# Optimization experiments

Measured on AMD Instinct MI355X. Metric: run time of the kernel, lower is better.

## Reference

```python
import math
import jax, jax.numpy as jnp
import numpy as np

N, B, C, H, K = 1024, 8, 512, 8, 5  # seq len, batch, d_model, heads, near_kth
NEG = -1.0e9


def setup_inputs() -> dict:
    key = jax.random.key(0)
    ks = jax.random.split(key, 10)
    s = 0.02
    return {
        "query": jax.random.normal(ks[0], (N, B, C), jnp.float32),
        "key_t": jax.random.normal(ks[1], (N, B, C), jnp.float32),
        "value": jax.random.normal(ks[2], (N, B, C), jnp.float32),
        "src_position": jax.random.normal(ks[3], (N, B, 3), jnp.float32),
        "tgt_position": jax.random.normal(ks[4], (N, B, 3), jnp.float32),
        # nn.MultiheadAttention params (in_proj split into q/k/v, plus out_proj)
        "Wq": jax.random.normal(ks[5], (C, C), jnp.float32) * s,
        "Wk": jax.random.normal(ks[6], (C, C), jnp.float32) * s,
        "Wv": jax.random.normal(ks[7], (C, C), jnp.float32) * s,
        "bq": jnp.zeros((C,), jnp.float32),
        "bk": jnp.zeros((C,), jnp.float32),
        "bv": jnp.zeros((C,), jnp.float32),
        "Wo": jax.random.normal(ks[8], (C, C), jnp.float32) * s,
        "bo": jnp.zeros((C,), jnp.float32),
    }


def reference(query, key_t, value, src_position, tgt_position,
              Wq, Wk, Wv, bq, bk, bv, Wo, bo):
    # --- 'nearby' positional mask ---------------------------------------
    # dist[b, tgt, src] = ||src_position[src,b] - tgt_position[tgt,b]||^2
    diff = src_position[None, :, :, :] - tgt_position[:, None, :, :]  # (Nt,Ns,B,3)
    dist = jnp.sum(diff * diff, axis=-1).transpose(2, 0, 1)           # (B,Nt,Ns)
    # torch: topk(dist, k=5, dim=1, largest=False) -> 5 nearest TARGETS per source
    _, idx = jax.lax.top_k(-dist.transpose(0, 2, 1), K)               # (B,Ns,K) tgt idx
    mask = jnp.full((B, N, N), NEG, jnp.float32)
    b_i = jnp.arange(B)[:, None, None]
    s_i = jnp.arange(N)[None, :, None]
    mask = mask.at[b_i, idx, s_i].set(0.0)                            # (B,Nt,Ns)

    # --- multihead attention (eval mode, dropout=0) ----------------------
    hd = C // H
    scale = 1.0 / math.sqrt(hd)
    q = ((query @ Wq.T + bq) * scale).reshape(N, B, H, hd)
    k = (key_t @ Wk.T + bk).reshape(N, B, H, hd)
    v = (value @ Wv.T + bv).reshape(N, B, H, hd)
    scores = jnp.einsum('tbhd,sbhd->bhts', q, k) + mask[:, None]      # (B,H,Nt,Ns)
    attn = jax.nn.softmax(scores, axis=-1)
    ctx = jnp.einsum('bhts,sbhd->tbhd', attn, v).reshape(N, B, C)
    out = ctx @ Wo.T + bo                                             # (N,B,C)
    attn_avg = attn.mean(axis=1)                                      # (B,Nt,Ns)
    return out, attn_avg
```

## Files before the change

### kernel.cpp

```cpp
#include <hip/hip_runtime.h>
#include <cstdint>
#include <cstddef>

#define NSEQ 1024
#define BATCH 8
#define CMODEL 512
#define NHEAD 8
#define HDIM 64
#define CAP 64
#define FLTMAX 3.402823466e+38f

typedef short bf16x8 __attribute__((ext_vector_type(8)));
typedef float f32x4 __attribute__((ext_vector_type(4)));
typedef unsigned short ushort8v __attribute__((ext_vector_type(8)));
typedef unsigned short ushort2v __attribute__((ext_vector_type(2)));

__device__ inline unsigned short f2bf(float f) {
    unsigned int u = __builtin_bit_cast(unsigned int, f);
    u += 0x7fffu + ((u >> 16) & 1u);
    return (unsigned short)(u >> 16);
}
__device__ inline float bf2f(unsigned short u) {
    return __builtin_bit_cast(float, (unsigned int)u << 16);
}

#define GLDS16(gsrc, ldst) \
    __builtin_amdgcn_global_load_lds((const __attribute__((address_space(1))) void*)(gsrc), \
                                     (__attribute__((address_space(3))) void*)(ldst), 16, 0, 0)

__global__ __launch_bounds__(256) void prep(const float* __restrict__ w0,
                                            const float* __restrict__ w1,
                                            const float* __restrict__ w2,
                                            const float* __restrict__ w3,
                                            const float* __restrict__ value,
                                            const float* __restrict__ tgtp,
                                            const float* __restrict__ srcp,
                                            unsigned short* __restrict__ o0,
                                            unsigned short* __restrict__ o1,
                                            unsigned short* __restrict__ o2,
                                            unsigned short* __restrict__ o3,
                                            unsigned int* __restrict__ zp,
                                            float* __restrict__ vm_raw,
                                            float* __restrict__ tgt_soa,
                                            float* __restrict__ src_soa) {
    const int bid = blockIdx.x;
    const int tid = threadIdx.x;
    if (bid < 512) {
        const int idx = bid * 256 + tid;
        const int seg = idx >> 15;
        const int c   = idx & 32767;
        const float* src = seg == 0 ? w0 : seg == 1 ? w1 : seg == 2 ? w2 : w3;
        unsigned short* dst = seg == 0 ? o0 : seg == 1 ? o1 : seg == 2 ? o2 : o3;
        const float4 v0 = *(const float4*)(src + (size_t)c * 8);
        const float4 v1 = *(const float4*)(src + (size_t)c * 8 + 4);
        ushort8v u;
        u[0] = f2bf(v0.x); u[1] = f2bf(v0.y); u[2] = f2bf(v0.z); u[3] = f2bf(v0.w);
        u[4] = f2bf(v1.x); u[5] = f2bf(v1.y); u[6] = f2bf(v1.z); u[7] = f2bf(v1.w);
        *(ushort8v*)(dst + (size_t)c * 8) = u;
        return;
    }
    if (bid < 544) {
        zp[(bid - 512) * 256 + tid] = 0u;
        return;
    }
    if (bid < 608) {
        const int cb = bid - 544;
        const int b = cb >> 3, cg = cb & 7;
        const int ts = tid >> 6, c = cg * 64 + (tid & 63);
        float s = 0.f;
        for (int i = 0; i < 256; ++i) {
            const int t = ts * 256 + i;
            s += value[((size_t)t * BATCH + b) * CMODEL + c];
        }
        __shared__ float sh[4][64];
        sh[ts][tid & 63] = s;
        __syncthreads();
        if (ts == 0)
            vm_raw[b * CMODEL + c] = sh[0][tid & 63] + sh[1][tid & 63] +
                                     sh[2][tid & 63] + sh[3][tid & 63];
        return;
    }
    const int tb = bid - 608;
    const int which = tb >> 3, b = tb & 7;
    const float* src = which == 0 ? tgtp : srcp;
    float* dst = which == 0 ? tgt_soa : src_soa;
    for (int t = tid; t < NSEQ; t += 256) {
        const float* p = src + ((size_t)t * BATCH + b) * 3;
        dst[(b * 3 + 0) * NSEQ + t] = p[0];
        dst[(b * 3 + 1) * NSEQ + t] = p[1];
        dst[(b * 3 + 2) * NSEQ + t] = p[2];
    }
}

__device__ inline void gemm_fp32A_body(const float* __restrict__ A,
                                       const unsigned short* __restrict__ Wbf,
                                       const float* __restrict__ bias,
                                       unsigned short* __restrict__ outp,
                                       float scale, int m0, int n0) {
    __shared__ __align__(16) unsigned short smem[3 * 8192];
    const int tid = threadIdx.x;
    const int l = tid & 63, w = tid >> 6;
    const int wr = (w >> 1) * 64, wc = (w & 1) * 64;
    const int lr = l & 15, g = l >> 4;

    f32x4 acc[4][4] = {};

    const int rowA = tid >> 2;
    const int slA  = tid & 3;
    const int sw   = (rowA >> 1) & 3;
    const float* aS0 = A + (size_t)(m0 + rowA) * CMODEL + slA * 8;
    const float* aS1 = aS0 + (size_t)64 * CMODEL;
    const int adst0 = rowA * 32 + (slA ^ sw) * 8;
    const int adst1 = adst0 + 64 * 32;
    const unsigned short* bS0 = Wbf + (size_t)(n0 + rowA) * CMODEL + (slA ^ sw) * 8;
    const unsigned short* bS1 = bS0 + (size_t)64 * CMODEL;
    const int wb = w * 512;

    float4 sets[2][4];

    auto LOADA = [&](int S, int k0) {
        sets[S][0] = *(const float4*)(aS0 + k0);
        sets[S][1] = *(const float4*)(aS0 + k0 + 4);
        sets[S][2] = *(const float4*)(aS1 + k0);
        sets[S][3] = *(const float4*)(aS1 + k0 + 4);
    };
    auto CVT_WRITE = [&](int S, int buf) {
        ushort8v u0, u1;
        u0[0] = f2bf(sets[S][0].x); u0[1] = f2bf(sets[S][0].y);
        u0[2] = f2bf(sets[S][0].z); u0[3] = f2bf(sets[S][0].w);
        u0[4] = f2bf(sets[S][1].x); u0[5] = f2bf(sets[S][1].y);
        u0[6] = f2bf(sets[S][1].z); u0[7] = f2bf(sets[S][1].w);
        u1[0] = f2bf(sets[S][2].x); u1[1] = f2bf(sets[S][2].y);
        u1[2] = f2bf(sets[S][2].z); u1[3] = f2bf(sets[S][2].w);
        u1[4] = f2bf(sets[S][3].x); u1[5] = f2bf(sets[S][3].y);
        u1[6] = f2bf(sets[S][3].z); u1[7] = f2bf(sets[S][3].w);
        unsigned short* bb = smem + buf * 8192;
        *(ushort8v*)(bb + adst0) = u0;
        *(ushort8v*)(bb + adst1) = u1;
    };
    auto STAGE_B = [&](int k0, int buf) {
        unsigned short* bb = smem + buf * 8192 + 4096;
        GLDS16(bS0 + k0, bb + wb);
        GLDS16(bS1 + k0, bb + 2048 + wb);
    };
    auto COMPUTE = [&](const unsigned short* base) {
        bf16x8 af[4], bg[4];
        #pragma unroll
        for (int i = 0; i < 4; ++i) {
            const int ra = wr + i * 16 + lr;
            af[i] = *(const bf16x8*)(base + ra * 32 + ((g ^ ((ra >> 1) & 3)) << 3));
        }
        #pragma unroll
        for (int j = 0; j < 4; ++j) {
            const int rb = wc + j * 16 + lr;
            bg[j] = *(const bf16x8*)(base + 4096 + rb * 32 + ((g ^ ((rb >> 1) & 3)) << 3));
        }
        #pragma unroll
        for (int i = 0; i < 4; ++i)
            #pragma unroll
            for (int j = 0; j < 4; ++j)
                acc[i][j] = __builtin_amdgcn_mfma_f32_16x16x32_bf16(af[i], bg[j], acc[i][j], 0, 0, 0);
    };

    LOADA(0, 0);
    LOADA(1, 32);
    STAGE_B(0, 0);
    STAGE_B(32, 1);
    CVT_WRITE(0, 0);
    LOADA(0, 64);

    #pragma unroll
    for (int t = 0; t < 13; ++t) {
        const int S = (t + 1) & 1;
        CVT_WRITE(S, (t + 1) % 3);
        LOADA(S, (t + 3) * 32);
        asm volatile("s_waitcnt vmcnt(10)" ::: "memory");
        asm volatile("s_waitcnt lgkmcnt(0)" ::: "memory");
        __builtin_amdgcn_s_barrier();
        STAGE_B((t + 2) * 32, (t + 2) % 3);
        COMPUTE(smem + (t % 3) * 8192);
    }
    CVT_WRITE(0, 2);
    asm volatile("s_waitcnt vmcnt(6)" ::: "memory");
    asm volatile("s_waitcnt lgkmcnt(0)" ::: "memory");
    __builtin_amdgcn_s_barrier();
    STAGE_B(15 * 32, 0);
    COMPUTE(smem + 1 * 8192);
    CVT_WRITE(1, 0);
    asm volatile("s_waitcnt vmcnt(2)" ::: "memory");
    asm volatile("s_waitcnt lgkmcnt(0)" ::: "memory");
    __builtin_amdgcn_s_barrier();
    COMPUTE(smem + 2 * 8192);
    asm volatile("s_waitcnt vmcnt(0)" ::: "memory");
    asm volatile("s_waitcnt lgkmcnt(0)" ::: "memory");
    __builtin_amdgcn_s_barrier();
    COMPUTE(smem + 0 * 8192);

    #pragma unroll
    for (int i = 0; i < 4; ++i) {
        #pragma unroll
        for (int j = 0; j < 4; ++j) {
            const int col = n0 + wc + j * 16 + lr;
            const float bcol = bias[col];
            #pragma unroll
            for (int r = 0; r < 4; ++r) {
                const int row = m0 + wr + i * 16 + g * 4 + r;
                const float val = (acc[i][j][r] + bcol) * scale;
                const int t = row >> 3, bb = row & 7;
                outp[((size_t)(bb * NSEQ + t)) * CMODEL + col] = f2bf(val);
            }
        }
    }
}

__global__ __launch_bounds__(256, 3) void mega(const float* __restrict__ Aq,
                                               const float* __restrict__ Ak,
                                               const float* __restrict__ Av,
                                               const unsigned short* __restrict__ Wq,
                                               const unsigned short* __restrict__ Wk,
                                               const unsigned short* __restrict__ Wv,
                                               const float* __restrict__ bq,
                                               const float* __restrict__ bk,
                                               const float* __restrict__ bv,
                                               unsigned short* __restrict__ oq,
                                               unsigned short* __restrict__ ok,
                                               unsigned short* __restrict__ ov,
                                               const float* __restrict__ src_soa,
                                               const float* __restrict__ tgt_soa,
                                               int* __restrict__ row_cnt,
                                               int* __restrict__ row_list,
                                               const float* __restrict__ vm_raw,
                                               float* __restrict__ vm) {
    const int p = blockIdx.x;

    if (p < 768) {
        const int logical = (p & 7) * 96 + (p >> 3);
        const int z = logical >> 8;
        const int r = logical & 255;
        const int m0 = (r >> 2) * 128, n0 = (r & 3) * 128;
        const float* A = z == 0 ? Aq : z == 1 ? Ak : Av;
        const unsigned short* W = z == 0 ? Wq : z == 1 ? Wk : Wv;
        const float* bi = z == 0 ? bq : z == 1 ? bk : bv;
        unsigned short* o = z == 0 ? oq : z == 1 ? ok : ov;
        const float sc = z == 0 ? 0.125f : 1.0f;
        gemm_fp32A_body(A, W, bi, o, sc, m0, n0);
        return;
    }

    if (p >= 2816) {
        const int bsel = p - 2816;
        const int c0 = threadIdx.x * 2;
        float s0 = 0.f, s1 = 0.f;
        const unsigned short* w0r = Wv + (size_t)c0 * CMODEL;
        const unsigned short* w1r = w0r + CMODEL;
        const float* vr = vm_raw + bsel * CMODEL;
        for (int k8 = 0; k8 < 64; ++k8) {
            const ushort8v w0 = *(const ushort8v*)(w0r + k8 * 8);
            const ushort8v w1 = *(const ushort8v*)(w1r + k8 * 8);
            const float4 va = *(const float4*)(vr + k8 * 8);
            const float4 vb = *(const float4*)(vr + k8 * 8 + 4);
            s0 += va.x * bf2f(w0[0]) + va.y * bf2f(w0[1]) + va.z * bf2f(w0[2]) + va.w * bf2f(w0[3])
                + vb.x * bf2f(w0[4]) + vb.y * bf2f(w0[5]) + vb.z * bf2f(w0[6]) + vb.w * bf2f(w0[7]);
            s1 += va.x * bf2f(w1[0]) + va.y * bf2f(w1[1]) + va.z * bf2f(w1[2]) + va.w * bf2f(w1[3])
                + vb.x * bf2f(w1[4]) + vb.y * bf2f(w1[5]) + vb.z * bf2f(w1[6]) + vb.w * bf2f(w1[7]);
        }
        vm[bsel * CMODEL + c0]     = s0 * (1.f / (float)NSEQ) + bv[c0];
        vm[bsel * CMODEL + c0 + 1] = s1 * (1.f / (float)NSEQ) + bv[c0 + 1];
        return;
    }

    const int w = threadIdx.x >> 6, lane = threadIdx.x & 63;
    const int wg = (p - 768) * 4 + w;
    const int s = wg & 1023, b = wg >> 10;

    const float* tx = tgt_soa + (b * 3 + 0) * NSEQ;
    const float* ty = tgt_soa + (b * 3 + 1) * NSEQ;
    const float* tz = tgt_soa + (b * 3 + 2) * NSEQ;
    const float sx = src_soa[(b * 3 + 0) * NSEQ + s];
    const float sy = src_soa[(b * 3 + 1) * NSEQ + s];
    const float sz = src_soa[(b * 3 + 2) * NSEQ + s];

    float dv[16];
    #pragma unroll
    for (int i = 0; i < 16; ++i) {
        const int t = i * 64 + lane;
        const float dx = tx[t] - sx;
        const float dy = ty[t] - sy;
        const float dz = tz[t] - sz;
        dv[i] = dx * dx + dy * dy + dz * dz;
    }

    #pragma unroll
    for (int k = 0; k < 5; ++k) {
        float bvv = FLTMAX;
        int   bii = 0x7fffffff;
        #pragma unroll
        for (int i = 0; i < 16; ++i) {
            if (dv[i] < bvv) { bvv = dv[i]; bii = i * 64 + lane; }
        }
        #pragma unroll
        for (int off = 1; off < 64; off <<= 1) {
            const float ov = __shfl_xor(bvv, off);
            const int   oi = __shfl_xor(bii, off);
            if (ov < bvv || (ov == bvv && oi < bii)) { bvv = ov; bii = oi; }
        }
        if (lane == (bii & 63)) {
            #pragma unroll
            for (int i = 0; i < 16; ++i)
                if (bii == i * 64 + lane) dv[i] = FLTMAX;
        }
        if (lane == 0) {
            const int pos = atomicAdd(&row_cnt[b * NSEQ + bii], 1);
            if (pos < CAP) row_list[((size_t)b * NSEQ + bii) * CAP + pos] = s;
        }
    }
}

__global__ __launch_bounds__(256, 3) void gemm_out(const unsigned short* __restrict__ Abf,
                                                   const unsigned short* __restrict__ Wbf,
                                                   const float* __restrict__ bias,
                                                   float* __restrict__ out) {
    __shared__ __align__(16) unsigned short smem[3 * 6144];
    const int p = blockIdx.x;
    const int logical = (p & 7) * 64 + (p >> 3);
    const int m0 = (logical >> 3) * 128, n0 = (logical & 7) * 64;

    const int tid = threadIdx.x;
    const int l = tid & 63, w = tid >> 6;
    const int wr = (w >> 1) * 64, wc = (w & 1) * 32;
    const int lr = l & 15, g = l >> 4;

    f32x4 acc[4][2] = {};

    const int rowX = tid >> 2;
    const int kg0  = (tid & 3) ^ ((rowX >> 1) & 3);
    const unsigned short* aS0 = Abf + (size_t)(m0 + rowX) * CMODEL + kg0 * 8;
    const unsigned short* aS1 = aS0 + (size_t)64 * CMODEL;
    const unsigned short* bS0 = Wbf + (size_t)(n0 + rowX) * CMODEL + kg0 * 8;
    const int wb = w * 512;

    auto STAGE = [&](int k0, int buf) {
        unsigned short* bb = smem + buf * 6144;
        GLDS16(aS0 + k0, bb + wb);
        GLDS16(aS1 + k0, bb + 2048 + wb);
        GLDS16(bS0 + k0, bb + 4096 + wb);
    };
    auto COMPUTE = [&](const unsigned short* base) {
        bf16x8 af[4], bg[2];
        #pragma unroll
        for (int i = 0; i < 4; ++i) {
            const int ra = wr + i * 16 + lr;
            af[i] = *(const bf16x8*)(base + ra * 32 + ((g ^ ((ra >> 1) & 3)) << 3));
        }
        #pragma unroll
        for (int j = 0; j < 2; ++j) {
            const int rb = wc + j * 16 + lr;
            bg[j] = *(const bf16x8*)(base + 4096 + rb * 32 + ((g ^ ((rb >> 1) & 3)) << 3));
        }
        #pragma unroll
        for (int i = 0; i < 4; ++i)
            #pragma unroll
            for (int j = 0; j < 2; ++j)
                acc[i][j] = __builtin_amdgcn_mfma_f32_16x16x32_bf16(af[i], bg[j], acc[i][j], 0, 0, 0);
    };

    STAGE(0, 0);
    STAGE(32, 1);

    int cur = 0;
    for (int t = 0; t < 15; ++t) {
        asm volatile("s_waitcnt vmcnt(3)" ::: "memory");
        __builtin_amdgcn_s_barrier();
        if (t < 14) {
            int nb = cur + 2; if (nb >= 3) nb -= 3;
            STAGE((t + 2) * 32, nb);
        }
        COMPUTE(smem + cur * 6144);
        ++cur; if (cur == 3) cur = 0;
    }
    asm volatile("s_waitcnt vmcnt(0)" ::: "memory");
    __builtin_amdgcn_s_barrier();
    COMPUTE(smem + cur * 6144);

    #pragma unroll
    for (int i = 0; i < 4; ++i) {
        #pragma unroll
        for (int j = 0; j < 2; ++j) {
            const int col = n0 + wc + j * 16 + lr;
            const float bcol = bias[col];
            #pragma unroll
            for (int r = 0; r < 4; ++r) {
                const int row = m0 + wr + i * 16 + g * 4 + r;
                out[(size_t)row * CMODEL + col] = acc[i][j][r] + bcol;
            }
        }
    }
}

__global__ __launch_bounds__(256) void sparse_attn(const unsigned short* __restrict__ q_ws,
                                                   const unsigned short* __restrict__ k_ws,
                                                   const unsigned short* __restrict__ v_ws,
                                                   const int* __restrict__ row_cnt,
                                                   const int* __restrict__ row_list,
                                                   const float* __restrict__ vm,
                                                   unsigned short* __restrict__ ctx,
                                                   float* __restrict__ attn_out) {
    const int t = blockIdx.x;
    const int b = blockIdx.y;
    const int tid = threadIdx.x;

    int cnt = row_cnt[b * NSEQ + t];
    if (cnt > CAP) cnt = CAP;

    float* arow = attn_out + ((size_t)b * NSEQ + t) * NSEQ;

    if (cnt == 0) {
        const float u = 1.f / (float)NSEQ;
        const float4 uv = {u, u, u, u};
        ((float4*)arow)[tid] = uv;
        for (int c = tid; c < CMODEL; c += 256)
            ctx[((size_t)t * BATCH + b) * CMODEL + c] = f2bf(vm[b * CMODEL + c]);
        return;
    }

    {
        const float4 zv = {0.f, 0.f, 0.f, 0.f};
        ((float4*)arow)[tid] = zv;
    }

    __shared__ float qs[CMODEL];
    __shared__ float esc[CAP][8];
    __shared__ float denom[8];
    __shared__ int   slist[CAP];

    if (tid < 8) denom[tid] = 0.f;
    if (tid < cnt) slist[tid] = row_list[((size_t)b * NSEQ + t) * CAP + tid];
    {
        const ushort2v qv = *(const ushort2v*)(q_ws + ((size_t)b * NSEQ + t) * CMODEL + tid * 2);
        qs[tid * 2] = bf2f(qv[0]); qs[tid * 2 + 1] = bf2f(qv[1]);
    }
    __syncthreads();

    const int wid = tid >> 6, lane = tid & 63;
    for (int i = wid; i < cnt; i += 4) {
        const int s = slist[i];
        const ushort8v kv = *(const ushort8v*)(k_ws + ((size_t)b * NSEQ + s) * CMODEL + lane * 8);
        const float* qrow = qs + lane * 8;
        float part = 0.f;
        #pragma unroll
        for (int j = 0; j < 8; ++j) part += qrow[j] * bf2f(kv[j]);
        part += __shfl_xor(part, 1);
        part += __shfl_xor(part, 2);
        part += __shfl_xor(part, 4);
        if ((lane & 7) == 0) {
            const int h = lane >> 3;
            const float e = __expf(part);
            esc[i][h] = e;
            atomicAdd(&denom[h], e);
        }
    }
    __syncthreads();

    for (int x = tid; x < cnt * 8; x += 256)
        esc[x >> 3][x & 7] /= denom[x & 7];
    __syncthreads();

    for (int i = tid; i < cnt; i += 256) {
        float pm = 0.f;
        #pragma unroll
        for (int h = 0; h < 8; ++h) pm += esc[i][h];
        arow[slist[i]] = pm * 0.125f;
    }

    const int c0 = tid * 2;
    const int h0 = c0 >> 6;
    float acc0 = 0.f, acc1 = 0.f;
    for (int i = 0; i < cnt; ++i) {
        const int s = slist[i];
        const float p = esc[i][h0];
        const ushort2v vv = *(const ushort2v*)(v_ws + ((size_t)b * NSEQ + s) * CMODEL + c0);
        acc0 += p * bf2f(vv[0]); acc1 += p * bf2f(vv[1]);
    }
    unsigned short* crow = ctx + ((size_t)t * BATCH + b) * CMODEL;
    ushort2v cv; cv[0] = f2bf(acc0); cv[1] = f2bf(acc1);
    *(ushort2v*)(crow + c0) = cv;
}

extern "C" void kernel_launch(void* const* d_in, const int* in_sizes, int n_in,
                              void* d_out, int out_size, void* d_ws, size_t ws_size,
                              hipStream_t stream) {
    (void)in_sizes; (void)n_in; (void)out_size; (void)ws_size;

    const float* query = (const float*)d_in[0];
    const float* key_t = (const float*)d_in[1];
    const float* value = (const float*)d_in[2];
    const float* srcp  = (const float*)d_in[3];
    const float* tgtp  = (const float*)d_in[4];
    const float* Wq    = (const float*)d_in[5];
    const float* Wk    = (const float*)d_in[6];
    const float* Wv    = (const float*)d_in[7];
    const float* bq    = (const float*)d_in[8];
    const float* bk    = (const float*)d_in[9];
    const float* bv    = (const float*)d_in[10];
    const float* Wo    = (const float*)d_in[11];
    const float* bo    = (const float*)d_in[12];

    float* out      = (float*)d_out;
    float* attn_out = out + (size_t)NSEQ * BATCH * CMODEL;

    const size_t NBC = (size_t)BATCH * NSEQ * CMODEL;
    const size_t WSZ = (size_t)CMODEL * CMODEL;
    unsigned short* q_ws  = (unsigned short*)d_ws;
    unsigned short* k_ws  = q_ws + NBC;
    unsigned short* v_ws  = k_ws + NBC;
    unsigned short* ctxbf = v_ws + NBC;
    unsigned short* wqbf  = ctxbf + NBC;
    unsigned short* wkbf  = wqbf + WSZ;
    unsigned short* wvbf  = wkbf + WSZ;
    unsigned short* wobf  = wvbf + WSZ;
    int*   row_cnt  = (int*)(wobf + WSZ);
    float* vm       = (float*)(row_cnt + BATCH * NSEQ);
    float* vm_raw   = vm + BATCH * CMODEL;
    float* tgt_soa  = vm_raw + BATCH * CMODEL;
    float* src_soa  = tgt_soa + (size_t)BATCH * 3 * NSEQ;
    int*   row_list = (int*)(src_soa + (size_t)BATCH * 3 * NSEQ);

    prep<<<624, 256, 0, stream>>>(Wq, Wk, Wv, Wo, value, tgtp, srcp,
                                  wqbf, wkbf, wvbf, wobf,
                                  (unsigned int*)row_cnt, vm_raw,
                                  tgt_soa, src_soa);

    mega<<<2824, 256, 0, stream>>>(query, key_t, value,
                                   wqbf, wkbf, wvbf,
                                   bq, bk, bv,
                                   q_ws, k_ws, v_ws,
                                   src_soa, tgt_soa, row_cnt, row_list,
                                   vm_raw, vm);

    sparse_attn<<<dim3(NSEQ, BATCH), 256, 0, stream>>>(q_ws, k_ws, v_ws, row_cnt,
                                                       row_list, vm, ctxbf, attn_out);

    gemm_out<<<512, 256, 0, stream>>>(ctxbf, wobf, bo, out);
}
```

Before: 98.11 us.

## Pre-convert Q/K/V activations to bf16 and split projection GEMM into own kernel

The fused mega kernel ran the QKV projection GEMM with fp32 activations converted to bf16 inside the main loop, alongside the top-k mask work. This change adds a separate elementwise pass, merged into the mask/top-k kernel, that converts query, key and value to bf16 in workspace. A new standalone GEMM kernel then stages both operands with direct global-to-LDS loads in a simpler triple-buffered loop. This removes register staging and conversion from the GEMM inner loop. In exchange it adds an extra kernel launch, an extra full read and write of the activations in bf16, and it no longer overlaps the GEMM with the top-k work.

```diff
diff --git a/kernel.cpp b/kernel.cpp
--- a/kernel.cpp
+++ b/kernel.cpp
@@ -28,21 +28,21 @@
     __builtin_amdgcn_global_load_lds((const __attribute__((address_space(1))) void*)(gsrc), \
                                      (__attribute__((address_space(3))) void*)(ldst), 16, 0, 0)
 
-__global__ __launch_bounds__(256) void prep(const float* __restrict__ w0,
-                                            const float* __restrict__ w1,
-                                            const float* __restrict__ w2,
-                                            const float* __restrict__ w3,
-                                            const float* __restrict__ value,
-                                            const float* __restrict__ tgtp,
-                                            const float* __restrict__ srcp,
-                                            unsigned short* __restrict__ o0,
-                                            unsigned short* __restrict__ o1,
-                                            unsigned short* __restrict__ o2,
-                                            unsigned short* __restrict__ o3,
-                                            unsigned int* __restrict__ zp,
-                                            float* __restrict__ vm_raw,
-                                            float* __restrict__ tgt_soa,
-                                            float* __restrict__ src_soa) {
+__global__ __launch_bounds__(256) void prepA(const float* __restrict__ w0,
+                                             const float* __restrict__ w1,
+                                             const float* __restrict__ w2,
+                                             const float* __restrict__ w3,
+                                             const float* __restrict__ value,
+                                             const float* __restrict__ tgtp,
+                                             const float* __restrict__ srcp,
+                                             unsigned short* __restrict__ o0,
+                                             unsigned short* __restrict__ o1,
+                                             unsigned short* __restrict__ o2,
+                                             unsigned short* __restrict__ o3,
+                                             unsigned int* __restrict__ zp,
+                                             float* __restrict__ vm_raw,
+                                             float* __restrict__ tgt_soa,
+                                             float* __restrict__ src_soa) {
     const int bid = blockIdx.x;
     const int tid = threadIdx.x;
     if (bid < 512) {
@@ -92,164 +92,26 @@
     }
 }
 
-__device__ inline void gemm_fp32A_body(const float* __restrict__ A,
-                                       const unsigned short* __restrict__ Wbf,
-                                       const float* __restrict__ bias,
-                                       unsigned short* __restrict__ outp,
-                                       float scale, int m0, int n0) {
-    __shared__ __align__(16) unsigned short smem[3 * 8192];
+__global__ __launch_bounds__(256) void megaB(const float* __restrict__ a0,
+                                             const float* __restrict__ a1,
+                                             const float* __restrict__ a2,
+                                             unsigned short* __restrict__ oa0,
+                                             unsigned short* __restrict__ oa1,
+                                             unsigned short* __restrict__ oa2,
+                                             const float* __restrict__ src_soa,
+                                             const float* __restrict__ tgt_soa,
+                                             int* __restrict__ row_cnt,
+                                             int* __restrict__ row_list,
+                                             const unsigned short* __restrict__ Wv,
+                                             const float* __restrict__ bv,
+                                             const float* __restrict__ vm_raw,
+                                             float* __restrict__ vm) {
+    const int p = blockIdx.x;
     const int tid = threadIdx.x;
-    const int l = tid & 63, w = tid >> 6;
-    const int wr = (w >> 1) * 64, wc = (w & 1) * 64;
-    const int lr = l & 15, g = l >> 4;
-
-    f32x4 acc[4][4] = {};
-
-    const int rowA = tid >> 2;
-    const int slA  = tid & 3;
-    const int sw   = (rowA >> 1) & 3;
-    const float* aS0 = A + (size_t)(m0 + rowA) * CMODEL + slA * 8;
-    const float* aS1 = aS0 + (size_t)64 * CMODEL;
-    const int adst0 = rowA * 32 + (slA ^ sw) * 8;
-    const int adst1 = adst0 + 64 * 32;
-    const unsigned short* bS0 = Wbf + (size_t)(n0 + rowA) * CMODEL + (slA ^ sw) * 8;
-    const unsigned short* bS1 = bS0 + (size_t)64 * CMODEL;
-    const int wb = w * 512;
-
-    float4 sets[2][4];
-
-    auto LOADA = [&](int S, int k0) {
-        sets[S][0] = *(const float4*)(aS0 + k0);
-        sets[S][1] = *(const float4*)(aS0 + k0 + 4);
-        sets[S][2] = *(const float4*)(aS1 + k0);
-        sets[S][3] = *(const float4*)(aS1 + k0 + 4);
-    };
-    auto CVT_WRITE = [&](int S, int buf) {
-        ushort8v u0, u1;
-        u0[0] = f2bf(sets[S][0].x); u0[1] = f2bf(sets[S][0].y);
-        u0[2] = f2bf(sets[S][0].z); u0[3] = f2bf(sets[S][0].w);
-        u0[4] = f2bf(sets[S][1].x); u0[5] = f2bf(sets[S][1].y);
-        u0[6] = f2bf(sets[S][1].z); u0[7] = f2bf(sets[S][1].w);
-        u1[0] = f2bf(sets[S][2].x); u1[1] = f2bf(sets[S][2].y);
-        u1[2] = f2bf(sets[S][2].z); u1[3] = f2bf(sets[S][2].w);
-        u1[4] = f2bf(sets[S][3].x); u1[5] = f2bf(sets[S][3].y);
-        u1[6] = f2bf(sets[S][3].z); u1[7] = f2bf(sets[S][3].w);
-        unsigned short* bb = smem + buf * 8192;
-        *(ushort8v*)(bb + adst0) = u0;
-        *(ushort8v*)(bb + adst1) = u1;
-    };
-    auto STAGE_B = [&](int k0, int buf) {
-        unsigned short* bb = smem + buf * 8192 + 4096;
-        GLDS16(bS0 + k0, bb + wb);
-        GLDS16(bS1 + k0, bb + 2048 + wb);
-    };
-    auto COMPUTE = [&](const unsigned short* base) {
-        bf16x8 af[4], bg[4];
-        #pragma unroll
-        for (int i = 0; i < 4; ++i) {
-            const int ra = wr + i * 16 + lr;
-            af[i] = *(const bf16x8*)(base + ra * 32 + ((g ^ ((ra >> 1) & 3)) << 3));
-        }
-        #pragma unroll
-        for (int j = 0; j < 4; ++j) {
-            const int rb = wc + j * 16 + lr;
-            bg[j] = *(const bf16x8*)(base + 4096 + rb * 32 + ((g ^ ((rb >> 1) & 3)) << 3));
-        }
-        #pragma unroll
-        for (int i = 0; i < 4; ++i)
-            #pragma unroll
-            for (int j = 0; j < 4; ++j)
-                acc[i][j] = __builtin_amdgcn_mfma_f32_16x16x32_bf16(af[i], bg[j], acc[i][j], 0, 0, 0);
-    };
-
-    LOADA(0, 0);
-    LOADA(1, 32);
-    STAGE_B(0, 0);
-    STAGE_B(32, 1);
-    CVT_WRITE(0, 0);
-    LOADA(0, 64);
-
-    #pragma unroll
-    for (int t = 0; t < 13; ++t) {
-        const int S = (t + 1) & 1;
-        CVT_WRITE(S, (t + 1) % 3);
-        LOADA(S, (t + 3) * 32);
-        asm volatile("s_waitcnt vmcnt(10)" ::: "memory");
-        asm volatile("s_waitcnt lgkmcnt(0)" ::: "memory");
-        __builtin_amdgcn_s_barrier();
-        STAGE_B((t + 2) * 32, (t + 2) % 3);
-        COMPUTE(smem + (t % 3) * 8192);
-    }
-    CVT_WRITE(0, 2);
-    asm volatile("s_waitcnt vmcnt(6)" ::: "memory");
-    asm volatile("s_waitcnt lgkmcnt(0)" ::: "memory");
-    __builtin_amdgcn_s_barrier();
-    STAGE_B(15 * 32, 0);
-    COMPUTE(smem + 1 * 8192);
-    CVT_WRITE(1, 0);
-    asm volatile("s_waitcnt vmcnt(2)" ::: "memory");
-    asm volatile("s_waitcnt lgkmcnt(0)" ::: "memory");
-    __builtin_amdgcn_s_barrier();
-    COMPUTE(smem + 2 * 8192);
-    asm volatile("s_waitcnt vmcnt(0)" ::: "memory");
-    asm volatile("s_waitcnt lgkmcnt(0)" ::: "memory");
-    __builtin_amdgcn_s_barrier();
-    COMPUTE(smem + 0 * 8192);
-
-    #pragma unroll
-    for (int i = 0; i < 4; ++i) {
-        #pragma unroll
-        for (int j = 0; j < 4; ++j) {
-            const int col = n0 + wc + j * 16 + lr;
-            const float bcol = bias[col];
-            #pragma unroll
-            for (int r = 0; r < 4; ++r) {
-                const int row = m0 + wr + i * 16 + g * 4 + r;
-                const float val = (acc[i][j][r] + bcol) * scale;
-                const int t = row >> 3, bb = row & 7;
-                outp[((size_t)(bb * NSEQ + t)) * CMODEL + col] = f2bf(val);
-            }
-        }
-    }
-}
-
-__global__ __launch_bounds__(256, 3) void mega(const float* __restrict__ Aq,
-                                               const float* __restrict__ Ak,
-                                               const float* __restrict__ Av,
-                                               const unsigned short* __restrict__ Wq,
-                                               const unsigned short* __restrict__ Wk,
-                                               const unsigned short* __restrict__ Wv,
-                                               const float* __restrict__ bq,
-                                               const float* __restrict__ bk,
-                                               const float* __restrict__ bv,
-                                               unsigned short* __restrict__ oq,
-                                               unsigned short* __restrict__ ok,
-                                               unsigned short* __restrict__ ov,
-                                               const float* __restrict__ src_soa,
-                                               const float* __restrict__ tgt_soa,
-                                               int* __restrict__ row_cnt,
-                                               int* __restrict__ row_list,
-                                               const float* __restrict__ vm_raw,
-                                               float* __restrict__ vm) {
-    const int p = blockIdx.x;
-
-    if (p < 768) {
-        const int logical = (p & 7) * 96 + (p >> 3);
-        const int z = logical >> 8;
-        const int r = logical & 255;
-        const int m0 = (r >> 2) * 128, n0 = (r & 3) * 128;
-        const float* A = z == 0 ? Aq : z == 1 ? Ak : Av;
-        const unsigned short* W = z == 0 ? Wq : z == 1 ? Wk : Wv;
-        const float* bi = z == 0 ? bq : z == 1 ? bk : bv;
-        unsigned short* o = z == 0 ? oq : z == 1 ? ok : ov;
-        const float sc = z == 0 ? 0.125f : 1.0f;
-        gemm_fp32A_body(A, W, bi, o, sc, m0, n0);
-        return;
-    }
-
-    if (p >= 2816) {
-        const int bsel = p - 2816;
-        const int c0 = threadIdx.x * 2;
+
+    if (p < 8) {
+        const int bsel = p;
+        const int c0 = tid * 2;
         float s0 = 0.f, s1 = 0.f;
         const unsigned short* w0r = Wv + (size_t)c0 * CMODEL;
         const unsigned short* w1r = w0r + CMODEL;
@@ -269,8 +131,23 @@
         return;
     }
 
-    const int w = threadIdx.x >> 6, lane = threadIdx.x & 63;
-    const int wg = (p - 768) * 4 + w;
+    if (p >= 2056) {
+        const unsigned int idx = (unsigned int)(p - 2056) * 256u + tid;
+        const unsigned int seg = idx >> 19;
+        const unsigned int c   = idx & 524287u;
+        const float* src = seg == 0 ? a0 : seg == 1 ? a1 : a2;
+        unsigned short* dst = seg == 0 ? oa0 : seg == 1 ? oa1 : oa2;
+        const float4 v0 = *(const float4*)(src + (size_t)c * 8);
+        const float4 v1 = *(const float4*)(src + (size_t)c * 8 + 4);
+        ushort8v u;
+        u[0] = f2bf(v0.x); u[1] = f2bf(v0.y); u[2] = f2bf(v0.z); u[3] = f2bf(v0.w);
+        u[4] = f2bf(v1.x); u[5] = f2bf(v1.y); u[6] = f2bf(v1.z); u[7] = f2bf(v1.w);
+        *(ushort8v*)(dst + (size_t)c * 8) = u;
+        return;
+    }
+
+    const int w = tid >> 6, lane = tid & 63;
+    const int wg = (p - 8) * 4 + w;
     const int s = wg & 1023, b = wg >> 10;
 
     const float* tx = tgt_soa + (b * 3 + 0) * NSEQ;
@@ -312,6 +189,106 @@
         if (lane == 0) {
             const int pos = atomicAdd(&row_cnt[b * NSEQ + bii], 1);
             if (pos < CAP) row_list[((size_t)b * NSEQ + bii) * CAP + pos] = s;
+        }
+    }
+}
+
+__global__ __launch_bounds__(256, 3) void gemm_proj(const unsigned short* __restrict__ Aq,
+                                                    const unsigned short* __restrict__ Ak,
+                                                    const unsigned short* __restrict__ Av,
+                                                    const unsigned short* __restrict__ Wq,
+                                                    const unsigned short* __restrict__ Wk,
+                                                    const unsigned short* __restrict__ Wv,
+                                                    const float* __restrict__ bq,
+                                                    const float* __restrict__ bk,
+                                                    const float* __restrict__ bv,
+                                                    unsigned short* __restrict__ oq,
+                                                    unsigned short* __restrict__ ok,
+                                                    unsigned short* __restrict__ ov) {
+    __shared__ __align__(16) unsigned short smem[3 * 8192];
+    const int p = blockIdx.x;
+    const int logical = (p & 7) * 96 + (p >> 3);
+    const int z = logical >> 8;
+    const int r = logical & 255;
+    const int m0 = (r >> 2) * 128, n0 = (r & 3) * 128;
+    const unsigned short* Abf = z == 0 ? Aq : z == 1 ? Ak : Av;
+    const unsigned short* Wbf = z == 0 ? Wq : z == 1 ? Wk : Wv;
+    const float* bias = z == 0 ? bq : z == 1 ? bk : bv;
+    unsigned short* outp = z == 0 ? oq : z == 1 ? ok : ov;
+    const float scale = z == 0 ? 0.125f : 1.0f;
+
+    const int tid = threadIdx.x;
+    const int l = tid & 63, w = tid >> 6;
+    const int wr = (w >> 1) * 64, wc = (w & 1) * 64;
+    const int lr = l & 15, g = l >> 4;
+
+    f32x4 acc[4][4] = {};
+
+    const int rowX = tid >> 2;
+    const int kg0  = (tid & 3) ^ ((rowX >> 1) & 3);
+    const unsigned short* aS0 = Abf + (size_t)(m0 + rowX) * CMODEL + kg0 * 8;
+    const unsigned short* aS1 = aS0 + (size_t)64 * CMODEL;
+    const unsigned short* bS0 = Wbf + (size_t)(n0 + rowX) * CMODEL + kg0 * 8;
+    const unsigned short* bS1 = bS0 + (size_t)64 * CMODEL;
+    const int wb = w * 512;
+
+    auto STAGE = [&](int k0, int buf) {
+        unsigned short* bb = smem + buf * 8192;
+        GLDS16(aS0 + k0, bb + wb);
+        GLDS16(aS1 + k0, bb + 2048 + wb);
+        GLDS16(bS0 + k0, bb + 4096 + wb);
+        GLDS16(bS1 + k0, bb + 6144 + wb);
+    };
+    auto COMPUTE = [&](const unsigned short* base) {
+        bf16x8 af[4], bg[4];
+        #pragma unroll
+        for (int i = 0; i < 4; ++i) {
+            const int ra = wr + i * 16 + lr;
+            af[i] = *(const bf16x8*)(base + ra * 32 + ((g ^ ((ra >> 1) & 3)) << 3));
+        }
+        #pragma unroll
+        for (int j = 0; j < 4; ++j) {
+            const int rb = wc + j * 16 + lr;
+            bg[j] = *(const bf16x8*)(base + 4096 + rb * 32 + ((g ^ ((rb >> 1) & 3)) << 3));
+        }
+        #pragma unroll
+        for (int i = 0; i < 4; ++i)
+            #pragma unroll
+            for (int j = 0; j < 4; ++j)
+                acc[i][j] = __builtin_amdgcn_mfma_f32_16x16x32_bf16(af[i], bg[j], acc[i][j], 0, 0, 0);
+    };
+
+    STAGE(0, 0);
+    STAGE(32, 1);
+
+    int cur = 0;
+    for (int t = 0; t < 15; ++t) {
+        asm volatile("s_waitcnt vmcnt(4)" ::: "memory");
+        __builtin_amdgcn_s_barrier();
+        if (t < 14) {
+            int nb = cur + 2; if (nb >= 3) nb -= 3;
+            STAGE((t + 2) * 32, nb);
+        }
+        COMPUTE(smem + cur * 8192);
+        ++cur; if (cur == 3) cur = 0;
+    }
+    asm volatile("s_waitcnt vmcnt(0)" ::: "memory");
+    __builtin_amdgcn_s_barrier();
+    COMPUTE(smem + cur * 8192);
+
+    #pragma unroll
+    for (int i = 0; i < 4; ++i) {
+        #pragma unroll
+        for (int j = 0; j < 4; ++j) {
+            const int col = n0 + wc + j * 16 + lr;
+            const float bcol = bias[col];
+            #pragma unroll
+            for (int rr = 0; rr < 4; ++rr) {
+                const int row = m0 + wr + i * 16 + g * 4 + rr;
+                const float val = (acc[i][j][rr] + bcol) * scale;
+                const int t = row >> 3, bb = row & 7;
+                outp[((size_t)(bb * NSEQ + t)) * CMODEL + col] = f2bf(val);
+            }
         }
     }
 }
@@ -514,7 +491,10 @@
     unsigned short* k_ws  = q_ws + NBC;
     unsigned short* v_ws  = k_ws + NBC;
     unsigned short* ctxbf = v_ws + NBC;
-    unsigned short* wqbf  = ctxbf + NBC;
+    unsigned short* qbf   = ctxbf + NBC;
+    unsigned short* kbf   = qbf + NBC;
+    unsigned short* vbf   = kbf + NBC;
+    unsigned short* wqbf  = vbf + NBC;
     unsigned short* wkbf  = wqbf + WSZ;
     unsigned short* wvbf  = wkbf + WSZ;
     unsigned short* wobf  = wvbf + WSZ;
@@ -525,17 +505,19 @@
     float* src_soa  = tgt_soa + (size_t)BATCH * 3 * NSEQ;
     int*   row_list = (int*)(src_soa + (size_t)BATCH * 3 * NSEQ);
 
-    prep<<<624, 256, 0, stream>>>(Wq, Wk, Wv, Wo, value, tgtp, srcp,
-                                  wqbf, wkbf, wvbf, wobf,
-                                  (unsigned int*)row_cnt, vm_raw,
-                                  tgt_soa, src_soa);
-
-    mega<<<2824, 256, 0, stream>>>(query, key_t, value,
-                                   wqbf, wkbf, wvbf,
-                                   bq, bk, bv,
-                                   q_ws, k_ws, v_ws,
-                                   src_soa, tgt_soa, row_cnt, row_list,
-                                   vm_raw, vm);
+    prepA<<<624, 256, 0, stream>>>(Wq, Wk, Wv, Wo, value, tgtp, srcp,
+                                   wqbf, wkbf, wvbf, wobf,
+                                   (unsigned int*)row_cnt, vm_raw,
+                                   tgt_soa, src_soa);
+
+    megaB<<<8200, 256, 0, stream>>>(query, key_t, value, qbf, kbf, vbf,
+                                    src_soa, tgt_soa, row_cnt, row_list,
+                                    wvbf, bv, vm_raw, vm);
+
+    gemm_proj<<<768, 256, 0, stream>>>(qbf, kbf, vbf,
+                                       wqbf, wkbf, wvbf,
+                                       bq, bk, bv,
+                                       q_ws, k_ws, v_ws);
 
     sparse_attn<<<dim3(NSEQ, BATCH), 256, 0, stream>>>(q_ws, k_ws, v_ws, row_cnt,
                                                        row_list, vm, ctxbf, attn_out);
```

Result: slower. 103.7 us (+5.7%).
